# Kernel tuning notes

Hardware: AMD Instinct MI355X
Metric: run time of the kernel (lower is better)

## Reference

```python
import jax, jax.numpy as jnp
import numpy as np

D = 768       # model dim
H = 12        # num heads
DH = 64       # hidden_dim per head (D == H*DH)
DT = 32       # time_dim
KTEMP = 1.0   # k_temperature
LN_EPS = 1e-5


def setup_inputs() -> dict:
    key = jax.random.key(0)
    ks = jax.random.split(key, 10)
    B, T = 2, 2048
    states = jax.random.normal(ks[0], (B, T, D), jnp.float32)
    attention_mask = jnp.ones((B, T), jnp.int32)
    s = 0.02
    Wq = jax.random.normal(ks[1], (H * DH, D), jnp.float32) * s
    Wk = jax.random.normal(ks[2], (H * DH, D), jnp.float32) * s
    bk = jax.random.normal(ks[3], (H * DH,), jnp.float32) * s
    Wv = jax.random.normal(ks[4], (H * DH, D), jnp.float32) * s
    bv = jnp.zeros((H * DH,), jnp.float32)           # V.bias zeroed in __init__
    Wo = jax.random.normal(ks[5], (D, H * DH), jnp.float32) * s
    bo = jnp.zeros((D,), jnp.float32)                # O.bias zeroed in __init__
    q_bias = jnp.zeros((H * DH,), jnp.float32)
    time_angle = jax.random.uniform(ks[6], (H, DT), jnp.float32) ** 10 + 1e-8
    head_time_delta = jax.random.uniform(ks[7], (H,), jnp.float32)
    ln_gamma = jnp.ones((D,), jnp.float32)
    ln_beta = jnp.zeros((D,), jnp.float32)
    return {"states": states, "attention_mask": attention_mask,
            "Wq": Wq, "Wk": Wk, "bk": bk, "Wv": Wv, "bv": bv,
            "Wo": Wo, "bo": bo, "q_bias": q_bias,
            "time_angle": time_angle, "head_time_delta": head_time_delta,
            "ln_gamma": ln_gamma, "ln_beta": ln_beta}


def reference(states, attention_mask, Wq, Wk, bk, Wv, bv, Wo, bo, q_bias,
              time_angle, head_time_delta, ln_gamma, ln_beta):
    B, T, _ = states.shape
    dtype = states.dtype
    mask = attention_mask.astype(dtype)[..., None, None]  # B T 1 1

    inv_sqrt_dh = 1.0 / np.sqrt(DH).astype(np.float32)

    def get_time(delta):
        # delta: [1,H,1] or scalar 0.0
        pos = jnp.arange(T, dtype=dtype)[:, None, None]     # T 1 1
        ang = (pos + delta) * time_angle[None]              # T H Dt
        c, s = jnp.cos(ang), jnp.sin(ang)
        return jnp.concatenate([c + s, c - s], axis=-1) * inv_sqrt_dh  # T H 2Dt

    # --- q path ---
    q = states @ Wq.T - jnp.exp(q_bias)                     # B T (H*Dh), Q has no bias
    q = jax.nn.sigmoid(q.reshape(B, T, H, DH)) / DH * mask  # B T H Dh
    time_q = get_time(head_time_delta[None, :, None])       # T H 2Dt (with delta)
    time_k = get_time(0.0)                                  # T H 2Dt
    q_timed = q.sum(-1, keepdims=True) * time_q             # B T H 2Dt
    # scores: B T(query) L(key) H -- the large materialized tensor
    scores = jnp.einsum('bthd,lhd->btlh', q_timed, time_k)

    # --- kv path ---
    k = (states @ Wk.T + bk).reshape(B, T, H, DH) / KTEMP * mask
    v = (states @ Wv.T + bv).reshape(B, T, H, DH)
    kv = jax.nn.softmax(k, axis=-1) * v                     # B T H Dh

    # --- aggregate ---
    loading = jnp.einsum('btlh,blhd->bthd', scores, kv).reshape(B, T, D)
    attn_out = loading @ Wo.T + bo

    # residual + layernorm (dropout is identity in eval)
    x = states + attn_out
    mu = x.mean(-1, keepdims=True)
    var = x.var(-1, keepdims=True)
    return (x - mu) * jax.lax.rsqrt(var + LN_EPS) * ln_gamma + ln_beta
```

## Files before the change

### kernel.cpp

```cpp
#include <hip/hip_runtime.h>
#include <math.h>
#include <stdint.h>

#define TT 2048
#define BB 2
#define DD 768
#define HH 12
#define DHH 64
#define DTT 32
#define NROW 4096

typedef float v4 __attribute__((ext_vector_type(4)));
typedef __attribute__((ext_vector_type(8))) short s8v;
typedef __attribute__((ext_vector_type(4))) float f4v;
typedef unsigned short u16;
typedef __attribute__((ext_vector_type(4))) unsigned short us4;

__device__ __forceinline__ u16 f2bf(float x) {
  unsigned u = __builtin_bit_cast(unsigned, x);
  u += 0x7fffu + ((u >> 16) & 1u);
  return (u16)(u >> 16);
}
__device__ __forceinline__ float bf2f(u16 b) {
  return __builtin_bit_cast(float, (unsigned)b << 16);
}
__device__ __forceinline__ float wave_sum(float v) {
#pragma unroll
  for (int m = 32; m > 0; m >>= 1) v += __shfl_xor(v, m, 64);
  return v;
}
__device__ __forceinline__ void gload16(const void* g, void* l) {
  __builtin_amdgcn_global_load_lds(
      (const __attribute__((address_space(1))) unsigned int*)g,
      (__attribute__((address_space(3))) unsigned int*)l, 16, 0, 0);
}
__device__ __forceinline__ void wait_vm3() {
  asm volatile("s_waitcnt vmcnt(3)" ::: "memory");
  __builtin_amdgcn_sched_barrier(0);
}
__device__ __forceinline__ void wait_vm0() {
  asm volatile("s_waitcnt vmcnt(0)" ::: "memory");
  __builtin_amdgcn_sched_barrier(0);
}
__device__ __forceinline__ void raw_barrier() {
  asm volatile("s_barrier" ::: "memory");
}
__device__ __forceinline__ int swz_col(int row, int col) {
  int ch = (col >> 3) & 3;
  return (col & ~24) | (((ch ^ ((row >> 1) & 3)) & 3) << 3);
}

__global__ __launch_bounds__(256) void prep(
    const float* __restrict__ tang, const float* __restrict__ hdelta,
    const float* __restrict__ s, const float* __restrict__ wq,
    const float* __restrict__ wk, const float* __restrict__ wv,
    const float* __restrict__ wo, u16* __restrict__ timeqb,
    u16* __restrict__ timekb, u16* __restrict__ sb, u16* __restrict__ wqb,
    u16* __restrict__ wkvb, u16* __restrict__ wob) {
  int bid = blockIdx.x;
  if (bid < 192) {
    int idx = bid * 256 + threadIdx.x;
    int d = idx & 31;
    int h = (idx >> 5) % HH;
    int tc = idx / (32 * HH);
    int t0 = tc * 16;
    float ang = tang[h * DTT + d];
    float ca, sa;
    sincosf(ang, &sa, &ca);
    float ck, sk, cq, sq;
    sincosf((float)t0 * ang, &sk, &ck);
    sincosf(((float)t0 + hdelta[h]) * ang, &sq, &cq);
#pragma unroll
    for (int j = 0; j < 16; ++j) {
      int t = t0 + j;
      timekb[t * DD + h * DHH + d]       = f2bf((ck + sk) * 0.125f);
      timekb[t * DD + h * DHH + d + DTT] = f2bf((ck - sk) * 0.125f);
      timeqb[t * DD + h * DHH + d]       = f2bf((cq + sq) * 0.125f);
      timeqb[t * DD + h * DHH + d + DTT] = f2bf((cq - sq) * 0.125f);
      float ck2 = ck * ca - sk * sa;
      sk = sk * ca + ck * sa;
      ck = ck2;
      float cq2 = cq * ca - sq * sa;
      sq = sq * ca + cq * sa;
      cq = cq2;
    }
    return;
  }
  int idx = (bid - 192) * 256 + threadIdx.x;
  int off = idx * 4;
  const float* src;
  u16* dst;
  int so, rr, cc;
  if (off < 3145728) {
    src = s; dst = sb; so = off; rr = so / 768; cc = so % 768;
  } else if (off < 3735552) {
    src = wq; dst = wqb; so = off - 3145728; rr = so / 768; cc = so % 768;
  } else if (off < 4325376) {
    src = wk; so = off - 3735552;
    int j = so / 768; cc = so - j * 768;
    int h = j >> 6, r = j & 63;
    dst = wkvb; rr = h * 128 + r;
  } else if (off < 4915200) {
    src = wv; so = off - 4325376;
    int j = so / 768; cc = so - j * 768;
    int h = j >> 6, r = j & 63;
    dst = wkvb; rr = h * 128 + 64 + r;
  } else {
    src = wo; dst = wob; so = off - 4915200; rr = so / 768; cc = so % 768;
  }
  int dof = rr * 768 + swz_col(rr, cc);
  v4 f = *(const v4*)&src[so];
  us4 o;
#pragma unroll
  for (int j = 0; j < 4; ++j) o[j] = f2bf(f[j]);
  *(us4*)&dst[dof] = o;
}

__global__ __launch_bounds__(256) void gemm_qkv_fused(
    const u16* __restrict__ A, const u16* __restrict__ Wqb,
    const u16* __restrict__ Wkvb, const float* __restrict__ qb,
    const float* __restrict__ bk, const float* __restrict__ bv,
    const int* __restrict__ amask, float* __restrict__ qsum,
    u16* __restrict__ kvb) {
  __shared__ __align__(16) u16 As[2][2176];
  __shared__ __align__(16) u16 Bs[2][4096];
  const int tid = threadIdx.x;
  const int l = tid & 63;
  const int w = tid >> 6;
  const int wr = w >> 1, wc = w & 1;
  const int bx = blockIdx.x;
  const bool isQ = bx < 6;
  const int i0 = blockIdx.y * 64;
  const u16* Bbase = isQ ? (Wqb + (size_t)bx * 128 * 768)
                         : (Wkvb + (size_t)(bx - 6) * 128 * 768);
  const int srow = tid >> 2, scol = (tid & 3) * 8;
  const u16* gA0 = A + (size_t)(i0 + srow) * 768 + scol;
  const u16* gB0 = Bbase + (size_t)srow * 768 + scol;
  const u16* gB1 = gB0 + (size_t)64 * 768;
  const int lo = tid * 8;
  f4v acc[2][4];
#pragma unroll
  for (int m = 0; m < 2; ++m)
#pragma unroll
    for (int n = 0; n < 4; ++n) acc[m][n] = (f4v){0.f, 0.f, 0.f, 0.f};

#define STAGE(kt, b)                       \
  do {                                     \
    int kb_ = (kt) << 5;                   \
    gload16(gA0 + kb_, &As[b][lo]);        \
    gload16(gB0 + kb_, &Bs[b][lo]);        \
    gload16(gB1 + kb_, &Bs[b][2048 + lo]); \
  } while (0)

  STAGE(0, 0);
  STAGE(1, 1);
  int aoff[2], boff[4];
#pragma unroll
  for (int m = 0; m < 2; ++m) {
    int row = wr * 32 + (l & 15) + m * 16;
    aoff[m] = row * 32 + (((l >> 4) ^ ((row >> 1) & 3)) << 3);
  }
#pragma unroll
  for (int n = 0; n < 4; ++n) {
    int row = wc * 64 + (l & 15) + n * 16;
    boff[n] = row * 32 + (((l >> 4) ^ ((row >> 1) & 3)) << 3);
  }
  int cb = 0;
  for (int kt = 0; kt < 24; ++kt) {
    if (kt < 23) wait_vm3();
    else wait_vm0();
    raw_barrier();
    s8v af[2], bf4[4];
#pragma unroll
    for (int m = 0; m < 2; ++m) af[m] = *(const s8v*)&As[cb][aoff[m]];
#pragma unroll
    for (int n = 0; n < 4; ++n) bf4[n] = *(const s8v*)&Bs[cb][boff[n]];
#pragma unroll
    for (int m = 0; m < 2; ++m)
#pragma unroll
      for (int n = 0; n < 4; ++n)
        acc[m][n] =
            __builtin_amdgcn_mfma_f32_16x16x32_bf16(af[m], bf4[n], acc[m][n], 0, 0, 0);
    raw_barrier();
    if (kt + 2 < 24) STAGE(kt + 2, cb);
    cb ^= 1;
  }
  __syncthreads();

  const int crow = i0 + wr * 32 + (l >> 4) * 4;
  if (isQ) {
    const int head = bx * 2 + wc;
    float eqb[4];
#pragma unroll
    for (int n = 0; n < 4; ++n)
      eqb[n] = expf(qb[head * 64 + n * 16 + (l & 15)]);
#pragma unroll
    for (int m = 0; m < 2; ++m)
#pragma unroll
      for (int r = 0; r < 4; ++r) {
        float ssum = 0.f;
#pragma unroll
        for (int n = 0; n < 4; ++n)
          ssum += 1.f / (1.f + expf(-(acc[m][n][r] - eqb[n])));
#pragma unroll
        for (int mm = 8; mm > 0; mm >>= 1) ssum += __shfl_xor(ssum, mm, 64);
        int row = crow + m * 16 + r;
        if ((l & 15) == 0)
          qsum[row * HH + head] = ssum * (float)amask[row] * (1.f / 64.f);
      }
  } else {
    const int head = bx - 6;
    u16* Ps = &As[0][0];
    if (wc == 0) {
#pragma unroll
      for (int m = 0; m < 2; ++m)
#pragma unroll
        for (int r = 0; r < 4; ++r) {
          int row = crow + m * 16 + r;
          float mk = (float)amask[row];
          float kv4[4];
#pragma unroll
          for (int n = 0; n < 4; ++n)
            kv4[n] = (acc[m][n][r] + bk[head * 64 + n * 16 + (l & 15)]) * mk;
          float mx = fmaxf(fmaxf(kv4[0], kv4[1]), fmaxf(kv4[2], kv4[3]));
#pragma unroll
          for (int mm = 8; mm > 0; mm >>= 1)
            mx = fmaxf(mx, __shfl_xor(mx, mm, 64));
          float e[4], es = 0.f;
#pragma unroll
          for (int n = 0; n < 4; ++n) { e[n] = expf(kv4[n] - mx); es += e[n]; }
#pragma unroll
          for (int mm = 8; mm > 0; mm >>= 1) es += __shfl_xor(es, mm, 64);
          float inv = 1.f / es;
          int lrow = wr * 32 + (l >> 4) * 4 + m * 16 + r;
#pragma unroll
          for (int n = 0; n < 4; ++n)
            Ps[lrow * 68 + n * 16 + (l & 15)] = f2bf(e[n] * inv);
        }
    }
    __syncthreads();
    if (wc == 1) {
#pragma unroll
      for (int m = 0; m < 2; ++m)
#pragma unroll
        for (int r = 0; r < 4; ++r) {
          int row = crow + m * 16 + r;
          int lrow = wr * 32 + (l >> 4) * 4 + m * 16 + r;
#pragma unroll
          for (int n = 0; n < 4; ++n) {
            int d = n * 16 + (l & 15);
            float p = bf2f(Ps[lrow * 68 + d]);
            float vv = acc[m][n][r] + bv[head * 64 + d];
            kvb[((size_t)row * HH + head) * 64 + d] = f2bf(p * vv);
          }
        }
    }
  }
}

__global__ __launch_bounds__(256) void calc_M(
    const u16* __restrict__ timekb, const u16* __restrict__ kvb,
    float* __restrict__ Mpart) {
  int blk = blockIdx.x;
  int split = blk & 15;
  int bh = blk >> 4;
  int b = bh / HH, h = bh % HH;
  __shared__ float Tk[64][68];
  __shared__ float Kv[64][68];
  int tid = threadIdx.x;
  int tx = tid & 15, ty = tid >> 4;
  float acc[4][4] = {};
  int t0 = split * 128;
  for (int tt = 0; tt < 128; tt += 64) {
#pragma unroll
    for (int p = 0; p < 4; ++p) {
      int f = tid + 256 * p;
      int r = f >> 4, c4 = (f & 15) << 2;
      int t = t0 + tt + r;
      us4 tk = *(const us4*)&timekb[(size_t)t * DD + h * DHH + c4];
      us4 kv = *(const us4*)&kvb[((size_t)(b * TT + t) * HH + h) * 64 + c4];
#pragma unroll
      for (int j = 0; j < 4; ++j) {
        Tk[r][c4 + j] = bf2f(tk[j]);
        Kv[r][c4 + j] = bf2f(kv[j]);
      }
    }
    __syncthreads();
#pragma unroll
    for (int kk = 0; kk < 64; ++kk) {
      v4 a = *(const v4*)&Tk[kk][ty * 4];
      v4 bv4 = *(const v4*)&Kv[kk][tx * 4];
#pragma unroll
      for (int r = 0; r < 4; ++r)
#pragma unroll
        for (int c = 0; c < 4; ++c) acc[r][c] += a[r] * bv4[c];
    }
    __syncthreads();
  }
#pragma unroll
  for (int r = 0; r < 4; ++r)
#pragma unroll
    for (int c = 0; c < 4; ++c)
      Mpart[(size_t)blk * 4096 + (tx * 4 + c) * 64 + (ty * 4 + r)] = acc[r][c];
}

__global__ __launch_bounds__(256) void reduce_M(
    const float* __restrict__ Mpart, u16* __restrict__ Mtb) {
  int idx = blockIdx.x * 256 + threadIdx.x;
  int bh = idx >> 12;
  int p = idx & 4095;
  float s = 0.f;
#pragma unroll
  for (int sp = 0; sp < 16; ++sp)
    s += Mpart[(size_t)((bh << 4) + sp) * 4096 + p];
  Mtb[(size_t)bh * 4096 + p] = f2bf(s);
}

__global__ __launch_bounds__(256) void calc_loading_mfma(
    const u16* __restrict__ timeqb, const u16* __restrict__ Mtb,
    const float* __restrict__ qsum, u16* __restrict__ loading) {
  const int bh = blockIdx.y;
  const int b = bh / HH, h = bh % HH;
  const int t0 = blockIdx.x * 128;
  __shared__ __align__(16) u16 Ms[64 * 72];
  for (int p = threadIdx.x; p < 4096; p += 256)
    Ms[(p >> 6) * 72 + (p & 63)] = Mtb[(size_t)bh * 4096 + p];
  __syncthreads();
  const int l = threadIdx.x & 63, w = threadIdx.x >> 6;
  f4v acc[2][4];
#pragma unroll
  for (int m = 0; m < 2; ++m)
#pragma unroll
    for (int n = 0; n < 4; ++n) acc[m][n] = (f4v){0.f, 0.f, 0.f, 0.f};
  const int arow = t0 + w * 32 + (l & 15);
  const int dcol = l & 15;
#pragma unroll
  for (int ks = 0; ks < 2; ++ks) {
    const int k0 = ks * 32 + (l >> 4) * 8;
    s8v af[2], bf4[4];
#pragma unroll
    for (int m = 0; m < 2; ++m)
      af[m] = *(const s8v*)&timeqb[(size_t)(arow + m * 16) * DD + h * DHH + k0];
#pragma unroll
    for (int n = 0; n < 4; ++n)
      bf4[n] = *(const s8v*)&Ms[(dcol + n * 16) * 72 + k0];
#pragma unroll
    for (int m = 0; m < 2; ++m)
#pragma unroll
      for (int n = 0; n < 4; ++n)
        acc[m][n] =
            __builtin_amdgcn_mfma_f32_16x16x32_bf16(af[m], bf4[n], acc[m][n], 0, 0, 0);
  }
  const int trow = t0 + w * 32 + (l >> 4) * 4;
  float qs[2][4];
#pragma unroll
  for (int m = 0; m < 2; ++m)
#pragma unroll
    for (int r = 0; r < 4; ++r)
      qs[m][r] = qsum[(b * TT + trow + m * 16 + r) * HH + h];
#pragma unroll
  for (int m = 0; m < 2; ++m)
#pragma unroll
    for (int n = 0; n < 4; ++n)
#pragma unroll
      for (int r = 0; r < 4; ++r) {
        int i = b * TT + trow + m * 16 + r;
        int col = h * DHH + n * 16 + (l & 15);
        loading[(size_t)i * DD + swz_col(i, col)] =
            f2bf(qs[m][r] * acc[m][n][r]);
      }
}

__global__ __launch_bounds__(256) void gemm_out(
    const u16* __restrict__ A, const u16* __restrict__ B, float* __restrict__ C,
    const float* __restrict__ bias, const float* __restrict__ res) {
  __shared__ __align__(16) u16 As[2][2176];
  __shared__ __align__(16) u16 Bs[2][4096];
  const int tid = threadIdx.x;
  const int l = tid & 63;
  const int w = tid >> 6;
  const int wr = w >> 1, wc = w & 1;
  const int i0 = blockIdx.y * 64, j0 = blockIdx.x * 128;
  const int srow = tid >> 2, scol = (tid & 3) * 8;
  const u16* gA0 = A + (size_t)(i0 + srow) * 768 + scol;
  const u16* gB0 = B + (size_t)(j0 + srow) * 768 + scol;
  const u16* gB1 = gB0 + (size_t)64 * 768;
  const int lo = tid * 8;
  f4v acc[2][4];
#pragma unroll
  for (int m = 0; m < 2; ++m)
#pragma unroll
    for (int n = 0; n < 4; ++n) acc[m][n] = (f4v){0.f, 0.f, 0.f, 0.f};
  STAGE(0, 0);
  STAGE(1, 1);
  int aoff[2], boff[4];
#pragma unroll
  for (int m = 0; m < 2; ++m) {
    int row = wr * 32 + (l & 15) + m * 16;
    aoff[m] = row * 32 + (((l >> 4) ^ ((row >> 1) & 3)) << 3);
  }
#pragma unroll
  for (int n = 0; n < 4; ++n) {
    int row = wc * 64 + (l & 15) + n * 16;
    boff[n] = row * 32 + (((l >> 4) ^ ((row >> 1) & 3)) << 3);
  }
  int cb = 0;
  for (int kt = 0; kt < 24; ++kt) {
    if (kt < 23) wait_vm3();
    else wait_vm0();
    raw_barrier();
    s8v af[2], bf4[4];
#pragma unroll
    for (int m = 0; m < 2; ++m) af[m] = *(const s8v*)&As[cb][aoff[m]];
#pragma unroll
    for (int n = 0; n < 4; ++n) bf4[n] = *(const s8v*)&Bs[cb][boff[n]];
#pragma unroll
    for (int m = 0; m < 2; ++m)
#pragma unroll
      for (int n = 0; n < 4; ++n)
        acc[m][n] =
            __builtin_amdgcn_mfma_f32_16x16x32_bf16(af[m], bf4[n], acc[m][n], 0, 0, 0);
    raw_barrier();
    if (kt + 2 < 24) STAGE(kt + 2, cb);
    cb ^= 1;
  }
  __syncthreads();
  const int crow = i0 + wr * 32 + (l >> 4) * 4;
  const int ccol = j0 + wc * 64 + (l & 15);
#pragma unroll
  for (int m = 0; m < 2; ++m)
#pragma unroll
    for (int n = 0; n < 4; ++n) {
      int col = ccol + n * 16;
      size_t base = (size_t)(crow + m * 16) * 768 + col;
#pragma unroll
      for (int r = 0; r < 4; ++r)
        C[base + (size_t)r * 768] =
            acc[m][n][r] + bias[col] + res[base + (size_t)r * 768];
    }
}

__global__ __launch_bounds__(256) void layernorm(
    const float* __restrict__ X, const float* __restrict__ gamma,
    const float* __restrict__ beta, float* __restrict__ out) {
  int i = blockIdx.x;
  const float* x = X + (size_t)i * 768;
  float vals[3];
  float s = 0.f, s2 = 0.f;
#pragma unroll
  for (int p = 0; p < 3; ++p) {
    float v = x[threadIdx.x + 256 * p];
    vals[p] = v;
    s += v;
    s2 += v * v;
  }
  s = wave_sum(s);
  s2 = wave_sum(s2);
  __shared__ float red[8];
  int w = threadIdx.x >> 6;
  if ((threadIdx.x & 63) == 0) {
    red[w] = s;
    red[4 + w] = s2;
  }
  __syncthreads();
  float stot = red[0] + red[1] + red[2] + red[3];
  float s2tot = red[4] + red[5] + red[6] + red[7];
  float mu = stot * (1.f / 768.f);
  float var = s2tot * (1.f / 768.f) - mu * mu;
  float rs = rsqrtf(var + 1e-5f);
#pragma unroll
  for (int p = 0; p < 3; ++p) {
    int j = threadIdx.x + 256 * p;
    out[(size_t)i * 768 + j] = (vals[p] - mu) * rs * gamma[j] + beta[j];
  }
}

extern "C" void kernel_launch(void* const* d_in, const int* in_sizes, int n_in,
                              void* d_out, int out_size, void* d_ws,
                              size_t ws_size, hipStream_t stream) {
  const float* states = (const float*)d_in[0];
  const int* amask    = (const int*)d_in[1];
  const float* Wq     = (const float*)d_in[2];
  const float* Wk     = (const float*)d_in[3];
  const float* bk     = (const float*)d_in[4];
  const float* Wv     = (const float*)d_in[5];
  const float* bv     = (const float*)d_in[6];
  const float* Wo     = (const float*)d_in[7];
  const float* bo     = (const float*)d_in[8];
  const float* qb     = (const float*)d_in[9];
  const float* tang   = (const float*)d_in[10];
  const float* hdelta = (const float*)d_in[11];
  const float* gamma  = (const float*)d_in[12];
  const float* beta   = (const float*)d_in[13];
  float* out = (float*)d_out;
  float* ws = (float*)d_ws;

  u16* timeqb = (u16*)(ws + 0);
  u16* timekb = (u16*)(ws + 786432);
  u16* Abf    = (u16*)(ws + 1572864);
  u16* Wqb    = (u16*)(ws + 3145728);
  u16* Wkvb   = (u16*)(ws + 3440640);
  u16* Wob    = (u16*)(ws + 4030464);
  float* qsum = ws + 4325376;
  u16* kvb    = (u16*)(ws + 4374528);
  float* Mpart= ws + 5160960;
  u16* Mtb    = (u16*)(ws + 6733824);
  u16* loadb  = (u16*)(ws + 6758400);
  float* xbuf = ws + 7544832;

  prep<<<5568, 256, 0, stream>>>(tang, hdelta, states, Wq, Wk, Wv, Wo, timeqb,
                                 timekb, Abf, Wqb, Wkvb, Wob);
  gemm_qkv_fused<<<dim3(18, 64), 256, 0, stream>>>(Abf, Wqb, Wkvb, qb, bk, bv,
                                                   amask, qsum, kvb);
  calc_M<<<384, 256, 0, stream>>>(timekb, kvb, Mpart);
  reduce_M<<<384, 256, 0, stream>>>(Mpart, Mtb);
  calc_loading_mfma<<<dim3(16, 24), 256, 0, stream>>>(timeqb, Mtb, qsum, loadb);
  gemm_out<<<dim3(6, 64), 256, 0, stream>>>(loadb, Wob, xbuf, bo, states);
  layernorm<<<4096, 256, 0, stream>>>(xbuf, gamma, beta, out);
}
```

Measured before the change: 91.83 us.

## Triple-buffer GEMM pipelines and double grid sizes for small kernels

The QKV and output GEMMs move from double to triple LDS buffering. The next stage's load is now issued right after the top barrier, which removes the second barrier per k-step. The output GEMM tile shrinks to 64x64, calc_M doubles its time splits to 32, and calc_loading uses 64-row blocks, all to launch more blocks and fill the CUs. In exchange the kernels use more LDS, Mpart needs a larger workspace, and reduce_M must sum twice as many partials.

Result: slower. 94.35 us (+2.7%).

```diff
diff --git a/kernel.cpp b/kernel.cpp
--- a/kernel.cpp
+++ b/kernel.cpp
@@ -36,6 +36,10 @@
 }
 __device__ __forceinline__ void wait_vm3() {
   asm volatile("s_waitcnt vmcnt(3)" ::: "memory");
+  __builtin_amdgcn_sched_barrier(0);
+}
+__device__ __forceinline__ void wait_vm2() {
+  asm volatile("s_waitcnt vmcnt(2)" ::: "memory");
   __builtin_amdgcn_sched_barrier(0);
 }
 __device__ __forceinline__ void wait_vm0() {
@@ -122,8 +126,8 @@
     const float* __restrict__ bk, const float* __restrict__ bv,
     const int* __restrict__ amask, float* __restrict__ qsum,
     u16* __restrict__ kvb) {
-  __shared__ __align__(16) u16 As[2][2176];
-  __shared__ __align__(16) u16 Bs[2][4096];
+  __shared__ __align__(16) u16 As[3][2176];
+  __shared__ __align__(16) u16 Bs[3][4096];
   const int tid = threadIdx.x;
   const int l = tid & 63;
   const int w = tid >> 6;
@@ -170,6 +174,7 @@
     if (kt < 23) wait_vm3();
     else wait_vm0();
     raw_barrier();
+    if (kt + 2 < 24) STAGE(kt + 2, (cb + 2) % 3);
     s8v af[2], bf4[4];
 #pragma unroll
     for (int m = 0; m < 2; ++m) af[m] = *(const s8v*)&As[cb][aoff[m]];
@@ -181,9 +186,7 @@
       for (int n = 0; n < 4; ++n)
         acc[m][n] =
             __builtin_amdgcn_mfma_f32_16x16x32_bf16(af[m], bf4[n], acc[m][n], 0, 0, 0);
-    raw_barrier();
-    if (kt + 2 < 24) STAGE(kt + 2, cb);
-    cb ^= 1;
+    cb = (cb == 2) ? 0 : cb + 1;
   }
   __syncthreads();
 
@@ -262,40 +265,37 @@
     const u16* __restrict__ timekb, const u16* __restrict__ kvb,
     float* __restrict__ Mpart) {
   int blk = blockIdx.x;
-  int split = blk & 15;
-  int bh = blk >> 4;
+  int split = blk & 31;
+  int bh = blk >> 5;
   int b = bh / HH, h = bh % HH;
   __shared__ float Tk[64][68];
   __shared__ float Kv[64][68];
   int tid = threadIdx.x;
   int tx = tid & 15, ty = tid >> 4;
   float acc[4][4] = {};
-  int t0 = split * 128;
-  for (int tt = 0; tt < 128; tt += 64) {
-#pragma unroll
-    for (int p = 0; p < 4; ++p) {
-      int f = tid + 256 * p;
-      int r = f >> 4, c4 = (f & 15) << 2;
-      int t = t0 + tt + r;
-      us4 tk = *(const us4*)&timekb[(size_t)t * DD + h * DHH + c4];
-      us4 kv = *(const us4*)&kvb[((size_t)(b * TT + t) * HH + h) * 64 + c4];
-#pragma unroll
-      for (int j = 0; j < 4; ++j) {
-        Tk[r][c4 + j] = bf2f(tk[j]);
-        Kv[r][c4 + j] = bf2f(kv[j]);
-      }
+  int t0 = split * 64;
+#pragma unroll
+  for (int p = 0; p < 4; ++p) {
+    int f = tid + 256 * p;
+    int r = f >> 4, c4 = (f & 15) << 2;
+    int t = t0 + r;
+    us4 tk = *(const us4*)&timekb[(size_t)t * DD + h * DHH + c4];
+    us4 kv = *(const us4*)&kvb[((size_t)(b * TT + t) * HH + h) * 64 + c4];
+#pragma unroll
+    for (int j = 0; j < 4; ++j) {
+      Tk[r][c4 + j] = bf2f(tk[j]);
+      Kv[r][c4 + j] = bf2f(kv[j]);
     }
-    __syncthreads();
-#pragma unroll
-    for (int kk = 0; kk < 64; ++kk) {
-      v4 a = *(const v4*)&Tk[kk][ty * 4];
-      v4 bv4 = *(const v4*)&Kv[kk][tx * 4];
-#pragma unroll
-      for (int r = 0; r < 4; ++r)
-#pragma unroll
-        for (int c = 0; c < 4; ++c) acc[r][c] += a[r] * bv4[c];
-    }
-    __syncthreads();
+  }
+  __syncthreads();
+#pragma unroll
+  for (int kk = 0; kk < 64; ++kk) {
+    v4 a = *(const v4*)&Tk[kk][ty * 4];
+    v4 bv4 = *(const v4*)&Kv[kk][tx * 4];
+#pragma unroll
+    for (int r = 0; r < 4; ++r)
+#pragma unroll
+      for (int c = 0; c < 4; ++c) acc[r][c] += a[r] * bv4[c];
   }
 #pragma unroll
   for (int r = 0; r < 4; ++r)
@@ -311,8 +311,8 @@
   int p = idx & 4095;
   float s = 0.f;
 #pragma unroll
-  for (int sp = 0; sp < 16; ++sp)
-    s += Mpart[(size_t)((bh << 4) + sp) * 4096 + p];
+  for (int sp = 0; sp < 32; ++sp)
+    s += Mpart[(size_t)((bh << 5) + sp) * 4096 + p];
   Mtb[(size_t)bh * 4096 + p] = f2bf(s);
 }
 
@@ -321,122 +321,116 @@
     const float* __restrict__ qsum, u16* __restrict__ loading) {
   const int bh = blockIdx.y;
   const int b = bh / HH, h = bh % HH;
-  const int t0 = blockIdx.x * 128;
+  const int t0 = blockIdx.x * 64;
   __shared__ __align__(16) u16 Ms[64 * 72];
   for (int p = threadIdx.x; p < 4096; p += 256)
     Ms[(p >> 6) * 72 + (p & 63)] = Mtb[(size_t)bh * 4096 + p];
   __syncthreads();
   const int l = threadIdx.x & 63, w = threadIdx.x >> 6;
-  f4v acc[2][4];
-#pragma unroll
-  for (int m = 0; m < 2; ++m)
-#pragma unroll
-    for (int n = 0; n < 4; ++n) acc[m][n] = (f4v){0.f, 0.f, 0.f, 0.f};
-  const int arow = t0 + w * 32 + (l & 15);
+  f4v acc[4];
+#pragma unroll
+  for (int n = 0; n < 4; ++n) acc[n] = (f4v){0.f, 0.f, 0.f, 0.f};
+  const int arow = t0 + w * 16 + (l & 15);
   const int dcol = l & 15;
 #pragma unroll
   for (int ks = 0; ks < 2; ++ks) {
     const int k0 = ks * 32 + (l >> 4) * 8;
-    s8v af[2], bf4[4];
-#pragma unroll
-    for (int m = 0; m < 2; ++m)
-      af[m] = *(const s8v*)&timeqb[(size_t)(arow + m * 16) * DD + h * DHH + k0];
+    s8v af, bf4[4];
+    af = *(const s8v*)&timeqb[(size_t)arow * DD + h * DHH + k0];
 #pragma unroll
     for (int n = 0; n < 4; ++n)
       bf4[n] = *(const s8v*)&Ms[(dcol + n * 16) * 72 + k0];
 #pragma unroll
-    for (int m = 0; m < 2; ++m)
-#pragma unroll
-      for (int n = 0; n < 4; ++n)
-        acc[m][n] =
-            __builtin_amdgcn_mfma_f32_16x16x32_bf16(af[m], bf4[n], acc[m][n], 0, 0, 0);
-  }
-  const int trow = t0 + w * 32 + (l >> 4) * 4;
-  float qs[2][4];
-#pragma unroll
-  for (int m = 0; m < 2; ++m)
-#pragma unroll
-    for (int r = 0; r < 4; ++r)
-      qs[m][r] = qsum[(b * TT + trow + m * 16 + r) * HH + h];
-#pragma unroll
-  for (int m = 0; m < 2; ++m)
-#pragma unroll
     for (int n = 0; n < 4; ++n)
-#pragma unroll
-      for (int r = 0; r < 4; ++r) {
-        int i = b * TT + trow + m * 16 + r;
-        int col = h * DHH + n * 16 + (l & 15);
-        loading[(size_t)i * DD + swz_col(i, col)] =
-            f2bf(qs[m][r] * acc[m][n][r]);
-      }
+      acc[n] = __builtin_amdgcn_mfma_f32_16x16x32_bf16(af, bf4[n], acc[n], 0, 0, 0);
+  }
+  const int trow = t0 + w * 16 + (l >> 4) * 4;
+  float qs[4];
+#pragma unroll
+  for (int r = 0; r < 4; ++r)
+    qs[r] = qsum[(b * TT + trow + r) * HH + h];
+#pragma unroll
+  for (int n = 0; n < 4; ++n)
+#pragma unroll
+    for (int r = 0; r < 4; ++r) {
+      int i = b * TT + trow + r;
+      int col = h * DHH + n * 16 + (l & 15);
+      loading[(size_t)i * DD + swz_col(i, col)] = f2bf(qs[r] * acc[n][r]);
+    }
 }
 
 __global__ __launch_bounds__(256) void gemm_out(
     const u16* __restrict__ A, const u16* __restrict__ B, float* __restrict__ C,
     const float* __restrict__ bias, const float* __restrict__ res) {
-  __shared__ __align__(16) u16 As[2][2176];
-  __shared__ __align__(16) u16 Bs[2][4096];
+  __shared__ __align__(16) u16 As[3][2048];
+  __shared__ __align__(16) u16 Bs[3][2048];
   const int tid = threadIdx.x;
   const int l = tid & 63;
   const int w = tid >> 6;
   const int wr = w >> 1, wc = w & 1;
-  const int i0 = blockIdx.y * 64, j0 = blockIdx.x * 128;
+  const int i0 = blockIdx.y * 64, j0 = blockIdx.x * 64;
   const int srow = tid >> 2, scol = (tid & 3) * 8;
   const u16* gA0 = A + (size_t)(i0 + srow) * 768 + scol;
   const u16* gB0 = B + (size_t)(j0 + srow) * 768 + scol;
-  const u16* gB1 = gB0 + (size_t)64 * 768;
   const int lo = tid * 8;
-  f4v acc[2][4];
+  f4v acc[2][2];
 #pragma unroll
   for (int m = 0; m < 2; ++m)
 #pragma unroll
-    for (int n = 0; n < 4; ++n) acc[m][n] = (f4v){0.f, 0.f, 0.f, 0.f};
-  STAGE(0, 0);
-  STAGE(1, 1);
-  int aoff[2], boff[4];
+    for (int n = 0; n < 2; ++n) acc[m][n] = (f4v){0.f, 0.f, 0.f, 0.f};
+
+#define STAGE2(kt, b)                 \
+  do {                                \
+    int kb_ = (kt) << 5;              \
+    gload16(gA0 + kb_, &As[b][lo]);   \
+    gload16(gB0 + kb_, &Bs[b][lo]);   \
+  } while (0)
+
+  STAGE2(0, 0);
+  STAGE2(1, 1);
+  int aoff[2], boff[2];
 #pragma unroll
   for (int m = 0; m < 2; ++m) {
     int row = wr * 32 + (l & 15) + m * 16;
     aoff[m] = row * 32 + (((l >> 4) ^ ((row >> 1) & 3)) << 3);
   }
 #pragma unroll
-  for (int n = 0; n < 4; ++n) {
-    int row = wc * 64 + (l & 15) + n * 16;
+  for (int n = 0; n < 2; ++n) {
+    int row = wc * 32 + (l & 15) + n * 16;
     boff[n] = row * 32 + (((l >> 4) ^ ((row >> 1) & 3)) << 3);
   }
   int cb = 0;
   for (int kt = 0; kt < 24; ++kt) {
-    if (kt < 23) wait_vm3();
+    if (kt < 23) wait_vm2();
     else wait_vm0();
     raw_barrier();
-    s8v af[2], bf4[4];
+    if (kt + 2 < 24) STAGE2(kt + 2, (cb + 2) % 3);
+    s8v af[2], bf4[2];
 #pragma unroll
     for (int m = 0; m < 2; ++m) af[m] = *(const s8v*)&As[cb][aoff[m]];
 #pragma unroll
-    for (int n = 0; n < 4; ++n) bf4[n] = *(const s8v*)&Bs[cb][boff[n]];
+    for (int n = 0; n < 2; ++n) bf4[n] = *(const s8v*)&Bs[cb][boff[n]];
 #pragma unroll
     for (int m = 0; m < 2; ++m)
 #pragma unroll
-      for (int n = 0; n < 4; ++n)
+      for (int n = 0; n < 2; ++n)
         acc[m][n] =
             __builtin_amdgcn_mfma_f32_16x16x32_bf16(af[m], bf4[n], acc[m][n], 0, 0, 0);
-    raw_barrier();
-    if (kt + 2 < 24) STAGE(kt + 2, cb);
-    cb ^= 1;
-  }
-  __syncthreads();
+    cb = (cb == 2) ? 0 : cb + 1;
+  }
   const int crow = i0 + wr * 32 + (l >> 4) * 4;
-  const int ccol = j0 + wc * 64 + (l & 15);
+  const int ccol = j0 + wc * 32 + (l & 15);
 #pragma unroll
   for (int m = 0; m < 2; ++m)
 #pragma unroll
-    for (int n = 0; n < 4; ++n) {
+    for (int n = 0; n < 2; ++n) {
       int col = ccol + n * 16;
       size_t base = (size_t)(crow + m * 16) * 768 + col;
 #pragma unroll
-      for (int r = 0; r < 4; ++r)
-        C[base + (size_t)r * 768] =
-            acc[m][n][r] + bias[col] + res[base + (size_t)r * 768];
+      for (int r = 0; r < 2 * 2; ++r)
+        if (r < 4)
+          C[base + (size_t)r * 768] =
+              acc[m][n][r] + bias[col] + res[base + (size_t)r * 768];
     }
 }
 
@@ -504,17 +498,17 @@
   float* qsum = ws + 4325376;
   u16* kvb    = (u16*)(ws + 4374528);
   float* Mpart= ws + 5160960;
-  u16* Mtb    = (u16*)(ws + 6733824);
-  u16* loadb  = (u16*)(ws + 6758400);
-  float* xbuf = ws + 7544832;
+  u16* Mtb    = (u16*)(ws + 8306688);
+  u16* loadb  = (u16*)(ws + 8331264);
+  float* xbuf = ws + 9117696;
 
   prep<<<5568, 256, 0, stream>>>(tang, hdelta, states, Wq, Wk, Wv, Wo, timeqb,
                                  timekb, Abf, Wqb, Wkvb, Wob);
   gemm_qkv_fused<<<dim3(18, 64), 256, 0, stream>>>(Abf, Wqb, Wkvb, qb, bk, bv,
                                                    amask, qsum, kvb);
-  calc_M<<<384, 256, 0, stream>>>(timekb, kvb, Mpart);
+  calc_M<<<768, 256, 0, stream>>>(timekb, kvb, Mpart);
   reduce_M<<<384, 256, 0, stream>>>(Mpart, Mtb);
-  calc_loading_mfma<<<dim3(16, 24), 256, 0, stream>>>(timeqb, Mtb, qsum, loadb);
-  gemm_out<<<dim3(6, 64), 256, 0, stream>>>(loadb, Wob, xbuf, bo, states);
+  calc_loading_mfma<<<dim3(32, 24), 256, 0, stream>>>(timeqb, Mtb, qsum, loadb);
+  gemm_out<<<dim3(12, 64), 256, 0, stream>>>(loadb, Wob, xbuf, bo, states);
   layernorm<<<4096, 256, 0, stream>>>(xbuf, gamma, beta, out);
 }
```
